# Kernel optimization log

Measured on AMD Instinct MI355X. Metric: run time of the kernel, lower is better.

## Reference

```python
import jax, jax.numpy as jnp
import numpy as np
import math

B, S, DIM = 2, 1024, 2048
H, QR, KVR = 16, 1536, 512
DN, DR, DV = 128, 64, 128
QKD = DN + DR  # 192


def rotate_half(x):
    x1, x2 = jnp.split(x, 2, axis=-1)
    return jnp.concatenate([-x2, x1], axis=-1)


def rmsnorm(x, w, eps=1e-6):
    var = jnp.mean(x * x, axis=-1, keepdims=True)
    return x * jax.lax.rsqrt(var + eps) * w


def setup_inputs() -> dict:
    key = jax.random.key(0)
    ks = jax.random.split(key, 8)
    sc = 0.02
    x = jax.random.normal(ks[0], (B, S, DIM), dtype=jnp.float32)
    # causal additive mask [B, S, S]
    causal = jnp.where(jnp.arange(S)[:, None] >= jnp.arange(S)[None, :], 0.0, -1e9).astype(jnp.float32)
    mask = jnp.broadcast_to(causal, (B, S, S))
    wq_a_w = jax.random.normal(ks[1], (QR, DIM), dtype=jnp.float32) * sc
    wq_a_b = jnp.zeros((QR,), dtype=jnp.float32)
    q_norm_w = jnp.ones((QR,), dtype=jnp.float32)
    wq_b_w = jax.random.normal(ks[2], (H * QKD, QR), dtype=jnp.float32) * sc
    wq_b_b = jnp.zeros((H * QKD,), dtype=jnp.float32)
    wkv_a_w = jax.random.normal(ks[3], (KVR + DR, DIM), dtype=jnp.float32) * sc
    wkv_a_b = jnp.zeros((KVR + DR,), dtype=jnp.float32)
    kv_norm_w = jnp.ones((KVR,), dtype=jnp.float32)
    wk_b_w = jax.random.normal(ks[4], (H * (DN + DV), KVR), dtype=jnp.float32) * sc
    wo_w = jax.random.normal(ks[5], (DIM, H * DV), dtype=jnp.float32) * sc
    wo_b = jnp.zeros((DIM,), dtype=jnp.float32)
    # RotaryEmbedding buffers for rope head dim DR
    inv_freq = 1.0 / (10000.0 ** (np.arange(0, DR, 2, dtype=np.float32) / DR))
    t = np.arange(S, dtype=np.float32)[:, None]
    freqs = t * inv_freq[None, :]
    freqs = np.concatenate([freqs, freqs], axis=-1)  # [S, DR]
    cos = jnp.asarray(np.cos(freqs), dtype=jnp.float32)
    sin = jnp.asarray(np.sin(freqs), dtype=jnp.float32)
    return {"x": x, "mask": mask, "wq_a_w": wq_a_w, "wq_a_b": wq_a_b,
            "q_norm_w": q_norm_w, "wq_b_w": wq_b_w, "wq_b_b": wq_b_b,
            "wkv_a_w": wkv_a_w, "wkv_a_b": wkv_a_b, "kv_norm_w": kv_norm_w,
            "wk_b_w": wk_b_w, "wo_w": wo_w, "wo_b": wo_b, "cos": cos, "sin": sin}


def reference(x, mask, wq_a_w, wq_a_b, q_norm_w, wq_b_w, wq_b_b,
              wkv_a_w, wkv_a_b, kv_norm_w, wk_b_w, wo_w, wo_b, cos, sin):
    bs, seq_len, _ = x.shape
    # Q path: low-rank down-proj -> RMSNorm -> up-proj
    q = x @ wq_a_w.T + wq_a_b                      # [b,s,QR]
    q = rmsnorm(q, q_norm_w)
    q = q @ wq_b_w.T + wq_b_b                      # [b,s,H*QKD]
    q = q.reshape(bs, seq_len, H, QKD)
    q_nope, q_pe = q[..., :DN], q[..., DN:]        # [b,s,h,DN], [b,s,h,DR]
    # KV path: joint down-proj, split latent and rope part
    kv_all = x @ wkv_a_w.T + wkv_a_b               # [b,s,KVR+DR]
    kv, k_pe = kv_all[..., :KVR], kv_all[..., KVR:]
    # RoPE (cos/sin broadcast over heads for q, directly for k_pe [b,s,DR])
    cos_q = cos[None, :seq_len, None, :]
    sin_q = sin[None, :seq_len, None, :]
    q_pe = q_pe * cos_q + rotate_half(q_pe) * sin_q
    k_pe = k_pe * cos[None, :seq_len, :] + rotate_half(k_pe) * sin[None, :seq_len, :]
    # weight absorption: wk_b weight viewed per head
    wkv_b = wk_b_w.reshape(H, DN + DV, KVR)
    q_abs = jnp.einsum('bshd,hdc->bshc', q_nope, wkv_b[:, :DN, :])  # [b,s,h,KVR]
    kvn = rmsnorm(kv, kv_norm_w)                   # latent cache contents [b,t,KVR]
    scores = (jnp.einsum('bshc,btc->bsht', q_abs, kvn)
              + jnp.einsum('bshr,btr->bsht', q_pe, k_pe)) / math.sqrt(QKD)
    scores = scores + mask[:, :, None, :]          # mask.unsqueeze(2)
    p = jax.nn.softmax(scores, axis=-1)            # [b,s,h,t]
    o = jnp.einsum('bsht,btc->bshc', p, kvn)       # attend over latent
    o = jnp.einsum('bshc,hdc->bshd', o, wkv_b[:, DN:, :])  # up-project to v_head_dim
    o = o.reshape(bs, seq_len, H * DV)
    return o @ wo_w.T + wo_b
```

## Files before the change

### kernel.cpp

```cpp
#include <hip/hip_runtime.h>
#include <hip/hip_bf16.h>
#include <math.h>

#define BB 2
#define SS 1024
#define DIM 2048
#define HH 16
#define QR 1536
#define KVR 512
#define DN 128
#define DR 64
#define DV 128
#define QKD 192
#define NT (BB*SS)

typedef __attribute__((ext_vector_type(8))) short bhalf8;
typedef __attribute__((ext_vector_type(4))) float f32x4;

__device__ __forceinline__ unsigned short f2b(float f) {
  union { float f; unsigned u; } v; v.f = f;
  unsigned r = v.u + 0x7fffu + ((v.u >> 16) & 1u);
  return (unsigned short)(r >> 16);
}
__device__ __forceinline__ float b2f(unsigned short h) {
  union { unsigned u; float f; } v; v.u = ((unsigned)h) << 16;
  return v.f;
}

__device__ __forceinline__ void gload16(const void* g, void* l) {
  __builtin_amdgcn_global_load_lds((const __attribute__((address_space(1))) void*)g,
                                   (__attribute__((address_space(3))) void*)l, 16, 0, 0);
}

__global__ void cvt_k(const float* __restrict__ in, unsigned short* __restrict__ out, long n4) {
  long i = (long)blockIdx.x * 256 + threadIdx.x;
  if (i >= n4) return;
  float4 v = ((const float4*)in)[i];
  ushort4 o; o.x = f2b(v.x); o.y = f2b(v.y); o.z = f2b(v.z); o.w = f2b(v.w);
  ((ushort4*)out)[i] = o;
}

__global__ void cvtall_k(const float* __restrict__ x,     unsigned short* __restrict__ xb,
                         const float* __restrict__ wqa,   unsigned short* __restrict__ wqab,
                         const float* __restrict__ wkva,  unsigned short* __restrict__ wkvab,
                         const float* __restrict__ wk,    unsigned short* __restrict__ wkT)
{
  long i = (long)blockIdx.x * 256 + threadIdx.x;
  const float* in; unsigned short* out; long j;
  if (i < 1048576)      { in = x;    out = xb;    j = i; }
  else if (i < 1835008) { in = wqa;  out = wqab;  j = i - 1048576; }
  else if (i < 2129920) { in = wkva; out = wkvab; j = i - 1835008; }
  else {
    j = i - 2129920;
    if (j >= 262144) return;
    long e = j * 4;
    int d = (int)(e & 127), c = (int)((e >> 7) & 511), h = (int)(e >> 16);
    ushort4 o;
    o.x = f2b(wk[((long)h * 256 + d + 0) * 512 + c]);
    o.y = f2b(wk[((long)h * 256 + d + 1) * 512 + c]);
    o.z = f2b(wk[((long)h * 256 + d + 2) * 512 + c]);
    o.w = f2b(wk[((long)h * 256 + d + 3) * 512 + c]);
    ((ushort4*)wkT)[j] = o;
    return;
  }
  float4 v = ((const float4*)in)[j];
  ushort4 o; o.x = f2b(v.x); o.y = f2b(v.y); o.z = f2b(v.z); o.w = f2b(v.w);
  ((ushort4*)out)[j] = o;
}

__global__ void cvt2_k(const float* __restrict__ wk, unsigned short* __restrict__ wkb,
                       const float* __restrict__ wo, unsigned short* __restrict__ wob)
{
  long i = (long)blockIdx.x * 256 + threadIdx.x;
  const float* in; unsigned short* out; long j;
  if (i < 524288) { in = wk; out = wkb; j = i; }
  else            { in = wo; out = wob; j = i - 524288; if (j >= 1048576) return; }
  float4 v = ((const float4*)in)[j];
  ushort4 o; o.x = f2b(v.x); o.y = f2b(v.y); o.z = f2b(v.z); o.w = f2b(v.w);
  ((ushort4*)out)[j] = o;
}

__global__ void kcT_k(const unsigned short* __restrict__ kc, unsigned short* __restrict__ kt) {
  int idx = blockIdx.x * 256 + threadIdx.x;
  int t = idx & 1023, c = (idx >> 10) & 511, b = idx >> 19;
  int csrc = c ^ ((t & 7) << 3);
  int kvd  = (t & 31) ^ (((c >> 1) & 3) << 3);
  kt[(((long)b * 32 + (t >> 5)) * 512 + c) * 32 + kvd] =
      kc[((long)b * SS + t) * 576 + csrc];
}

template<int OBF>
__global__ __launch_bounds__(256) void gemm_mfma(
    const unsigned short* __restrict__ A, int lda, long sA,
    const unsigned short* __restrict__ B, int ldb, long sB,
    void* __restrict__ C, int ldc, long sC,
    int M, int N, int K, const float* __restrict__ bias)
{
  const int bx = blockIdx.x, by = blockIdx.y, bz = blockIdx.z;
  const int m0 = by * 128, n0 = bx * 128;
  A += (long)bz * sA;
  B += (long)bz * sB;

  __shared__ unsigned short As[4096];
  __shared__ unsigned short Bs[4096];
  const int tid = threadIdx.x, l = tid & 63, w = tid >> 6;
  const int wr = w >> 1, wc = w & 1;
  const int rA = l >> 2;
  const int c8 = (((l & 3) ^ ((l >> 2) & 3)) << 3);

  f32x4 acc[4][4] = {};

  const unsigned short* Ab0 = A + (long)(m0 + w * 16 + rA) * lda + c8;
  const unsigned short* Ab1 = Ab0 + (long)64 * lda;
  int nb0 = n0 + w * 16 + rA;      if (nb0 > N - 1) nb0 = N - 1;
  int nb1 = n0 + 64 + w * 16 + rA; if (nb1 > N - 1) nb1 = N - 1;
  const unsigned short* Bb0 = B + (long)nb0 * ldb + c8;
  const unsigned short* Bb1 = B + (long)nb1 * ldb + c8;

  const int ko = (((l >> 4) ^ (l & 3)) << 3);

  for (int k0 = 0; k0 < K; k0 += 32) {
    gload16(Ab0 + k0, &As[w * 512]);
    gload16(Ab1 + k0, &As[(w + 4) * 512]);
    gload16(Bb0 + k0, &Bs[w * 512]);
    gload16(Bb1 + k0, &Bs[(w + 4) * 512]);
    __syncthreads();
    bhalf8 af[4], bv[4];
#pragma unroll
    for (int m = 0; m < 4; ++m) {
      af[m] = *(const bhalf8*)&As[(wr * 64 + m * 16 + (l & 15)) * 32 + ko];
      bv[m] = *(const bhalf8*)&Bs[(wc * 64 + m * 16 + (l & 15)) * 32 + ko];
    }
#pragma unroll
    for (int m = 0; m < 4; ++m)
#pragma unroll
      for (int n = 0; n < 4; ++n)
        acc[m][n] = __builtin_amdgcn_mfma_f32_16x16x32_bf16(af[m], bv[n], acc[m][n], 0, 0, 0);
    __syncthreads();
  }

  const int ro = (l >> 4) << 2;
  const int co = l & 15;
#pragma unroll
  for (int m = 0; m < 4; ++m) {
    int row = m0 + wr * 64 + m * 16 + ro;
#pragma unroll
    for (int n = 0; n < 4; ++n) {
      int col = n0 + wc * 64 + n * 16 + co;
      if (col < N) {
        float bvl = bias ? bias[col] : 0.f;
#pragma unroll
        for (int r = 0; r < 4; ++r) {
          float v = acc[m][n][r] + bvl;
          long off = (long)bz * sC + (long)(row + r) * ldc + col;
          if (OBF) ((unsigned short*)C)[off] = f2b(v);
          else     ((float*)C)[off] = v;
        }
      }
    }
  }
}

template<int OBF, int ROPE, int SPLIT>
__global__ __launch_bounds__(256) void gemm64(
    const unsigned short* __restrict__ A, int lda, long sA,
    const unsigned short* __restrict__ B, int ldb, long sB,
    void* __restrict__ C, int ldc, long sC,
    int M, int N, int K, const float* __restrict__ bias,
    unsigned short* __restrict__ qcat, const float* __restrict__ cosT,
    const float* __restrict__ sinT,
    float* __restrict__ C2, const float* __restrict__ bias2)
{
  const int bx = blockIdx.x, by = blockIdx.y, bz = blockIdx.z;
  const int m0 = by * 64, n0 = bx * 128;
  A += (long)bz * sA;
  B += (long)bz * sB;

  __shared__ unsigned short As[2048];
  __shared__ unsigned short Bs[4096];
  const int tid = threadIdx.x, l = tid & 63, w = tid >> 6;
  const int rA = l >> 2;
  const int c8 = (((l & 3) ^ ((l >> 2) & 3)) << 3);

  f32x4 acc[8] = {};

  const unsigned short* Ab0 = A + (long)(m0 + w * 16 + rA) * lda + c8;
  int nb0 = n0 + w * 16 + rA;      if (nb0 > N - 1) nb0 = N - 1;
  int nb1 = n0 + 64 + w * 16 + rA; if (nb1 > N - 1) nb1 = N - 1;
  const unsigned short* Bb0 = B + (long)nb0 * ldb + c8;
  const unsigned short* Bb1 = B + (long)nb1 * ldb + c8;

  const int ko = (((l >> 4) ^ (l & 3)) << 3);

  for (int k0 = 0; k0 < K; k0 += 32) {
    gload16(Ab0 + k0, &As[w * 512]);
    gload16(Bb0 + k0, &Bs[w * 512]);
    gload16(Bb1 + k0, &Bs[(w + 4) * 512]);
    __syncthreads();
    bhalf8 af = *(const bhalf8*)&As[(w * 16 + (l & 15)) * 32 + ko];
    bhalf8 bv[8];
#pragma unroll
    for (int n = 0; n < 8; ++n)
      bv[n] = *(const bhalf8*)&Bs[(n * 16 + (l & 15)) * 32 + ko];
#pragma unroll
    for (int n = 0; n < 8; ++n)
      acc[n] = __builtin_amdgcn_mfma_f32_16x16x32_bf16(af, bv[n], acc[n], 0, 0, 0);
    __syncthreads();
  }

  const int ro = (l >> 4) << 2;
  const int co = l & 15;
#pragma unroll
  for (int r = 0; r < 4; ++r) {
    int row = m0 + w * 16 + ro + r;
    float v[8];
#pragma unroll
    for (int n = 0; n < 8; ++n) {
      int col = n0 + n * 16 + co;
      float bv2 = 0.f;
      if (SPLIT) bv2 = (col < QR) ? bias[col] : ((col < QR + 576) ? bias2[col - QR] : 0.f);
      else if (bias && col < N) bv2 = bias[col];
      v[n] = acc[n][r] + bv2;
    }
    if (ROPE) {
      int s = row & (SS - 1);
#pragma unroll
      for (int n = 0; n < 8; ++n) {
        int col0 = n0 + n * 16;
        int cm0 = col0 % 192;
        if (cm0 < 128) {
          ((unsigned short*)C)[(long)row * ldc + col0 + co] = f2b(v[n]);
        } else if (cm0 == 128 || cm0 == 144) {
          int d = cm0 - 128 + co;
          float cl = cosT[s * DR + d],      sl = sinT[s * DR + d];
          float ch = cosT[s * DR + d + 32], sh = sinT[s * DR + d + 32];
          float o_lo = v[n] * cl - v[n + 2] * sl;
          float o_hi = v[n + 2] * ch + v[n] * sh;
          unsigned short* qp = qcat + ((long)(col0 / 192) * NT + row) * 576 + 512;
          qp[d]      = f2b(o_lo);
          qp[d + 32] = f2b(o_hi);
        }
      }
    } else if (SPLIT) {
#pragma unroll
      for (int n = 0; n < 8; ++n) {
        int col = n0 + n * 16 + co;
        if (col < QR)            ((float*)C)[(long)row * ldc + col] = v[n];
        else if (col < QR + 576) C2[(long)row * 576 + (col - QR)] = v[n];
      }
    } else {
#pragma unroll
      for (int n = 0; n < 8; ++n) {
        int col = n0 + n * 16 + co;
        if (col < N) {
          long off = (long)bz * sC + (long)row * ldc + col;
          if (OBF) ((unsigned short*)C)[off] = f2b(v[n]);
          else     ((float*)C)[off] = v[n];
        }
      }
    }
  }
}

template<int SWZ>
__global__ void rmsnorm_k(const float* __restrict__ in, int ldin,
                          unsigned short* __restrict__ out, int ldout,
                          const float* __restrict__ w, int N) {
  long row = blockIdx.x;
  const float* x = in + row * ldin;
  unsigned short* y = out + row * ldout;
  float ss = 0.f;
  for (int i = threadIdx.x; i < N; i += 256) { float u = x[i]; ss += u * u; }
  for (int o = 32; o > 0; o >>= 1) ss += __shfl_down(ss, o);
  __shared__ float red[4];
  int lane = threadIdx.x & 63, wid = threadIdx.x >> 6;
  if (lane == 0) red[wid] = ss;
  __syncthreads();
  float r = rsqrtf((red[0] + red[1] + red[2] + red[3]) / (float)N + 1e-6f);
  int sw = SWZ ? (((int)row & 7) << 3) : 0;
  for (int i = threadIdx.x; i < N; i += 256) y[i ^ sw] = f2b(x[i] * r * w[i]);
}

__global__ void rope_k_k(const float* __restrict__ kv, unsigned short* __restrict__ kc,
                         const float* __restrict__ cosT, const float* __restrict__ sinT) {
  int idx = blockIdx.x * 256 + threadIdx.x;
  int d = idx & 31, t = idx >> 5, s = t & (SS - 1);
  const float* p = kv + (long)t * 576 + 512;
  float x1 = p[d], x2 = p[d + 32];
  float c1 = cosT[s * DR + d],      s1 = sinT[s * DR + d];
  float c2 = cosT[s * DR + 32 + d], s2 = sinT[s * DR + 32 + d];
  unsigned short* o = kc + (long)t * 576;
  int sw = (t & 7) << 3;
  o[(512 + d) ^ sw]      = f2b(x1 * c1 - x2 * s1);
  o[(512 + d + 32) ^ sw] = f2b(x2 * c2 + x1 * s2);
}

__global__ __launch_bounds__(256) void flash_k(
    const unsigned short* __restrict__ qcat,
    const unsigned short* __restrict__ kcb,
    const unsigned short* __restrict__ kct,
    unsigned short* __restrict__ omid)
{
  __shared__ __align__(16) char lds[73728];
  char* Kl = lds;
  char* Vl = lds + 36864;
  char* Pl = lds + 69632;

  const int bid = blockIdx.x;
  const int qt = 15 - (bid >> 5);
  const int bh = bid & 31;
  const int b = bh & 1, h = bh >> 1;
  const int tid = threadIdx.x, l = tid & 63, w = tid >> 6;
  const int lo = l & 15, hi = l >> 4;

  const unsigned short* qrow =
      qcat + ((long)h * NT + b * SS + qt * 64 + w * 16 + lo) * 576 + hi * 8;
  bhalf8 qf[18];
#pragma unroll
  for (int ks = 0; ks < 18; ++ks) qf[ks] = *(const bhalf8*)(qrow + ks * 32);

  f32x4 po[32] = {};
  float mrow[4] = {-1e30f, -1e30f, -1e30f, -1e30f};
  float lrow[4] = {0.f, 0.f, 0.f, 0.f};
  const float sc = 0.07216878364870323f;
  char* Pwv = Pl + w * 1024;

  const char* ksrc = (const char*)kcb + (long)b * SS * 1152;
  const char* vsrc = (const char*)kct + (long)b * 32 * 32768;
  const int smax = 2 * qt + 1;

  for (int st = 0; st <= smax; ++st) {
#pragma unroll
    for (int i = 0; i < 9; ++i) {
      int off = (w + i * 4) * 1024 + l * 16;
      gload16(ksrc + off, Kl + off);
    }
#pragma unroll
    for (int i = 0; i < 8; ++i) {
      int off = (w + i * 4) * 1024 + l * 16;
      gload16(vsrc + off, Vl + off);
    }
    __syncthreads();

    f32x4 sa[2] = {};
    __builtin_amdgcn_s_setprio(1);
#pragma unroll
    for (int ks = 0; ks < 18; ++ks) {
#pragma unroll
      for (int n = 0; n < 2; ++n) {
        int kv = n * 16 + lo;
        bhalf8 kf = *(const bhalf8*)(Kl + kv * 1152 + (((ks * 4 + hi) ^ (kv & 7)) << 4));
        sa[n] = __builtin_amdgcn_mfma_f32_16x16x32_bf16(qf[ks], kf, sa[n], 0, 0, 0);
      }
    }
    __builtin_amdgcn_s_setprio(0);
    if (st >= 2 * qt) {
      const int kv0 = st * 32;
#pragma unroll
      for (int n = 0; n < 2; ++n) {
        int kvg = kv0 + n * 16 + lo;
#pragma unroll
        for (int r = 0; r < 4; ++r) {
          int qg = qt * 64 + w * 16 + hi * 4 + r;
          sa[n][r] = (kvg > qg) ? -1e30f : sa[n][r] * sc;
        }
      }
    } else {
#pragma unroll
      for (int n = 0; n < 2; ++n)
#pragma unroll
        for (int r = 0; r < 4; ++r) sa[n][r] *= sc;
    }
    float pmax[4];
#pragma unroll
    for (int r = 0; r < 4; ++r) {
      float v = fmaxf(sa[0][r], sa[1][r]);
      v = fmaxf(v, __shfl_xor(v, 1));
      v = fmaxf(v, __shfl_xor(v, 2));
      v = fmaxf(v, __shfl_xor(v, 4));
      v = fmaxf(v, __shfl_xor(v, 8));
      pmax[r] = v;
    }
    bool need = false;
#pragma unroll
    for (int r = 0; r < 4; ++r) need |= (pmax[r] > mrow[r] + 8.f);
    if (__any(need)) {
#pragma unroll
      for (int r = 0; r < 4; ++r) {
        float mn = fmaxf(mrow[r], pmax[r]);
        float fac = __expf(mrow[r] - mn);
        mrow[r] = mn;
        lrow[r] *= fac;
#pragma unroll
        for (int nv = 0; nv < 32; ++nv) po[nv][r] *= fac;
      }
    }
    float rs[4] = {0.f, 0.f, 0.f, 0.f};
#pragma unroll
    for (int n = 0; n < 2; ++n)
#pragma unroll
      for (int r = 0; r < 4; ++r) {
        float p = __expf(sa[n][r] - mrow[r]);
        sa[n][r] = p;
        rs[r] += p;
      }
#pragma unroll
    for (int r = 0; r < 4; ++r) {
      float v = rs[r];
      v += __shfl_xor(v, 1); v += __shfl_xor(v, 2);
      v += __shfl_xor(v, 4); v += __shfl_xor(v, 8);
      lrow[r] += v;
    }
#pragma unroll
    for (int n = 0; n < 2; ++n)
#pragma unroll
      for (int r = 0; r < 4; ++r) {
        int q = hi * 4 + r, kv = n * 16 + lo;
        *(unsigned short*)(Pwv + q * 64 + ((kv * 2) ^ ((q & 3) << 4))) = f2b(sa[n][r]);
      }
    bhalf8 pa = *(const bhalf8*)(Pwv + lo * 64 + ((hi * 16) ^ ((lo & 3) << 4)));
    __builtin_amdgcn_s_setprio(1);
#pragma unroll
    for (int nv = 0; nv < 32; ++nv) {
      int vc = nv * 16 + lo;
      bhalf8 vb = *(const bhalf8*)(Vl + vc * 64 + ((hi ^ ((vc >> 1) & 3)) << 4));
      po[nv] = __builtin_amdgcn_mfma_f32_16x16x32_bf16(pa, vb, po[nv], 0, 0, 0);
    }
    __builtin_amdgcn_s_setprio(0);
    __syncthreads();
    ksrc += 36864; vsrc += 32768;
  }

  unsigned short* orow = omid + ((long)h * NT + b * SS + qt * 64) * 512;
  float inv[4];
#pragma unroll
  for (int r = 0; r < 4; ++r) inv[r] = 1.f / lrow[r];
#pragma unroll
  for (int nv = 0; nv < 32; ++nv)
#pragma unroll
    for (int r = 0; r < 4; ++r) {
      int q = w * 16 + hi * 4 + r;
      orow[(long)q * 512 + nv * 16 + lo] = f2b(po[nv][r] * inv[r]);
    }
}

extern "C" void kernel_launch(void* const* d_in, const int* in_sizes, int n_in,
                              void* d_out, int out_size, void* d_ws, size_t ws_size,
                              hipStream_t stream) {
  const float* x        = (const float*)d_in[0];
  const float* wq_a_w   = (const float*)d_in[2];
  const float* wq_a_b   = (const float*)d_in[3];
  const float* q_norm_w = (const float*)d_in[4];
  const float* wq_b_w   = (const float*)d_in[5];
  const float* wq_b_b   = (const float*)d_in[6];
  const float* wkv_a_w  = (const float*)d_in[7];
  const float* wkv_a_b  = (const float*)d_in[8];
  const float* kv_norm_w= (const float*)d_in[9];
  const float* wk_b_w   = (const float*)d_in[10];
  const float* wo_w     = (const float*)d_in[11];
  const float* wo_bias  = (const float*)d_in[12];
  const float* cosT     = (const float*)d_in[13];
  const float* sinT     = (const float*)d_in[14];
  float* out = (float*)d_out;

  char* W = (char*)d_ws;
  unsigned short* kcatb  = (unsigned short*)(W + 0);
  unsigned short* kcatT  = (unsigned short*)(W + 2359296);
  unsigned short* qcat   = (unsigned short*)(W + 4456448);
  unsigned short* o_mid  = (unsigned short*)(W + 42205184);
  unsigned short* xb     = (unsigned short*)(W + 4456448);
  unsigned short* wqa_b  = (unsigned short*)(W + 12845056);
  unsigned short* wkva_b = (unsigned short*)(W + 19136512);
  float*          kv_f32 = (float*)        (W + 21495808);
  unsigned short* qb     = (unsigned short*)(W + 42205184);
  unsigned short* wkT_b  = (unsigned short*)(W + 54788096);
  float*          qn_f32 = (float*)        (W + 56885248);
  unsigned short* wqb_b  = (unsigned short*)(W + 56885248);
  unsigned short* qnb    = (unsigned short*)(W + 69468160);
  unsigned short* wkb_b  = (unsigned short*)(W + 4456448);
  unsigned short* ohead  = (unsigned short*)(W + 8650752);
  unsigned short* wo_b16 = (unsigned short*)(W + 17039360);

  cvtall_k<<<9344, 256, 0, stream>>>(x, xb, wq_a_w, wqa_b, wkv_a_w, wkva_b, wk_b_w, wkT_b);

  gemm64<0,0,1><<<dim3(17, NT/64, 1), 256, 0, stream>>>(
      xb, DIM, 0, wqa_b, DIM, 0, qn_f32, QR, 0, NT, QR + 576, DIM, wq_a_b,
      nullptr, nullptr, nullptr, kv_f32, wkv_a_b);

  rmsnorm_k<1><<<NT, 256, 0, stream>>>(kv_f32, 576, kcatb, 576, kv_norm_w, KVR);
  rope_k_k<<<256, 256, 0, stream>>>(kv_f32, kcatb, cosT, sinT);
  kcT_k<<<4096, 256, 0, stream>>>(kcatb, kcatT);

  rmsnorm_k<0><<<NT, 256, 0, stream>>>(qn_f32, QR, qnb, QR, q_norm_w, QR);
  cvt_k<<<4608, 256, 0, stream>>>(wq_b_w, wqb_b, (long)3072 * QR / 4);
  gemm64<1,1,0><<<dim3(3072/128, NT/64, 1), 256, 0, stream>>>(
      qnb, QR, 0, wqb_b, QR, 0, qb, 3072, 0, NT, 3072, QR, wq_b_b,
      qcat, cosT, sinT, nullptr, nullptr);

  gemm_mfma<1><<<dim3(4, NT/128, 16), 256, 0, stream>>>(
      qb, 3072, QKD, wkT_b, DN, (long)KVR * DN,
      qcat, 576, (long)NT * 576, NT, KVR, DN, nullptr);

  flash_k<<<512, 256, 0, stream>>>(qcat, kcatb, kcatT, o_mid);

  cvt2_k<<<6144, 256, 0, stream>>>(wk_b_w, wkb_b, wo_w, wo_b16);

  gemm64<1,0,0><<<dim3(1, NT/64, 16), 256, 0, stream>>>(
      o_mid, KVR, (long)NT * KVR,
      wkb_b + (long)DN * KVR, KVR, (long)256 * KVR,
      ohead, HH * DV, DV, NT, DV, KVR, nullptr,
      nullptr, nullptr, nullptr, nullptr, nullptr);

  gemm64<0,0,0><<<dim3(DIM/128, NT/64, 1), 256, 0, stream>>>(
      ohead, 2048, 0, wo_b16, 2048, 0, out, DIM, 0, NT, DIM, 2048, wo_bias,
      nullptr, nullptr, nullptr, nullptr, nullptr);
}
```

Baseline: 333.9 us.

## Double-buffer K tiles in LDS and read V fragments directly from global

The flash attention kernel now prefetches the next K tile into a second LDS buffer while the current tile is being computed, which removes the load-then-barrier stall at the top of each iteration. V is no longer staged through LDS. Each wave loads its V fragments straight from the transposed latent buffer in global memory, in groups of eight, and the XOR swizzle in the transpose kernel is dropped to match. The cost is extra global and L2 traffic, because every wave re-reads the same V data, plus higher register pressure from the eight-entry fragment arrays.

Result: slower. 431.2 us (+29.1%).

```diff
diff --git a/kernel.cpp b/kernel.cpp
--- a/kernel.cpp
+++ b/kernel.cpp
@@ -84,8 +84,7 @@
   int idx = blockIdx.x * 256 + threadIdx.x;
   int t = idx & 1023, c = (idx >> 10) & 511, b = idx >> 19;
   int csrc = c ^ ((t & 7) << 3);
-  int kvd  = (t & 31) ^ (((c >> 1) & 3) << 3);
-  kt[(((long)b * 32 + (t >> 5)) * 512 + c) * 32 + kvd] =
+  kt[(((long)b * 32 + (t >> 5)) * 512 + c) * 32 + (t & 31)] =
       kc[((long)b * SS + t) * 576 + csrc];
 }
 
@@ -301,10 +300,10 @@
     const unsigned short* __restrict__ kct,
     unsigned short* __restrict__ omid)
 {
-  __shared__ __align__(16) char lds[73728];
-  char* Kl = lds;
-  char* Vl = lds + 36864;
-  char* Pl = lds + 69632;
+  __shared__ __align__(16) char lds[77824];
+  char* K0 = lds;
+  char* K1 = lds + 36864;
+  char* Pl = lds + 73728;
 
   const int bid = blockIdx.x;
   const int qt = 15 - (bid >> 5);
@@ -329,18 +328,25 @@
   const char* vsrc = (const char*)kct + (long)b * 32 * 32768;
   const int smax = 2 * qt + 1;
 
+#pragma unroll
+  for (int i = 0; i < 9; ++i) {
+    int off = (w + i * 4) * 1024 + l * 16;
+    gload16(ksrc + off, K0 + off);
+  }
+  __syncthreads();
+
+  char* Kc = K0;
+  char* Kn = K1;
+
   for (int st = 0; st <= smax; ++st) {
-#pragma unroll
-    for (int i = 0; i < 9; ++i) {
-      int off = (w + i * 4) * 1024 + l * 16;
-      gload16(ksrc + off, Kl + off);
-    }
-#pragma unroll
-    for (int i = 0; i < 8; ++i) {
-      int off = (w + i * 4) * 1024 + l * 16;
-      gload16(vsrc + off, Vl + off);
-    }
-    __syncthreads();
+    if (st < smax) {
+      const char* kn = ksrc + 36864;
+#pragma unroll
+      for (int i = 0; i < 9; ++i) {
+        int off = (w + i * 4) * 1024 + l * 16;
+        gload16(kn + off, Kn + off);
+      }
+    }
 
     f32x4 sa[2] = {};
     __builtin_amdgcn_s_setprio(1);
@@ -349,7 +355,7 @@
 #pragma unroll
       for (int n = 0; n < 2; ++n) {
         int kv = n * 16 + lo;
-        bhalf8 kf = *(const bhalf8*)(Kl + kv * 1152 + (((ks * 4 + hi) ^ (kv & 7)) << 4));
+        bhalf8 kf = *(const bhalf8*)(Kc + kv * 1152 + (((ks * 4 + hi) ^ (kv & 7)) << 4));
         sa[n] = __builtin_amdgcn_mfma_f32_16x16x32_bf16(qf[ks], kf, sa[n], 0, 0, 0);
       }
     }
@@ -421,13 +427,20 @@
     bhalf8 pa = *(const bhalf8*)(Pwv + lo * 64 + ((hi * 16) ^ ((lo & 3) << 4)));
     __builtin_amdgcn_s_setprio(1);
 #pragma unroll
-    for (int nv = 0; nv < 32; ++nv) {
-      int vc = nv * 16 + lo;
-      bhalf8 vb = *(const bhalf8*)(Vl + vc * 64 + ((hi ^ ((vc >> 1) & 3)) << 4));
-      po[nv] = __builtin_amdgcn_mfma_f32_16x16x32_bf16(pa, vb, po[nv], 0, 0, 0);
+    for (int g = 0; g < 4; ++g) {
+      bhalf8 vb[8];
+#pragma unroll
+      for (int j = 0; j < 8; ++j) {
+        int vc = (g * 8 + j) * 16 + lo;
+        vb[j] = *(const bhalf8*)(vsrc + (long)vc * 64 + hi * 16);
+      }
+#pragma unroll
+      for (int j = 0; j < 8; ++j)
+        po[g * 8 + j] = __builtin_amdgcn_mfma_f32_16x16x32_bf16(pa, vb[j], po[g * 8 + j], 0, 0, 0);
     }
     __builtin_amdgcn_s_setprio(0);
     __syncthreads();
+    { char* t = Kc; Kc = Kn; Kn = t; }
     ksrc += 36864; vsrc += 32768;
   }
 
```
